# Optimization experiments

Measured on AMD Instinct MI355X. Metric: run time of the kernel, lower is better.

## Reference

```python
import jax, jax.numpy as jnp
import numpy as np

EPS = 1e-5  # torch BatchNorm1d default eps

def _bn(y, gamma, beta):
    # training-mode BatchNorm1d over batch axis (biased variance), per timestep
    mu = jnp.mean(y, axis=0, keepdims=True)
    var = jnp.mean((y - mu) ** 2, axis=0, keepdims=True)
    return gamma * (y - mu) * jax.lax.rsqrt(var + EPS) + beta

def setup_inputs() -> dict:
    key = jax.random.key(0)
    ks = jax.random.split(key, 16)
    T, B, I, H = 512, 64, 512, 512
    s = 1.0 / np.sqrt(H)
    def w(k, shape):
        return jax.random.uniform(k, shape, jnp.float32, -s, s)
    return {
        "x": jax.random.normal(ks[0], (T, B, I), jnp.float32),
        "h0": jnp.zeros((1, B, H), jnp.float32),
        "W_z_w": w(ks[1], (H, H)), "W_z_b": w(ks[2], (H,)),
        "U_z_w": w(ks[3], (H, I)), "U_z_b": w(ks[4], (H,)),
        "W_r_w": w(ks[5], (H, H)), "W_r_b": w(ks[6], (H,)),
        "U_r_w": w(ks[7], (H, I)), "U_r_b": w(ks[8], (H,)),
        "W_h_w": w(ks[9], (H, H)), "W_h_b": w(ks[10], (H,)),
        "U_h_w": w(ks[11], (H, I)), "U_h_b": w(ks[12], (H,)),
        "bn_gamma": jnp.ones((H,), jnp.float32),
        "bn_beta": jnp.zeros((H,), jnp.float32),
    }

def reference(x, h0, W_z_w, W_z_b, U_z_w, U_z_b, W_r_w, W_r_b, U_r_w, U_r_b,
              W_h_w, W_h_b, U_h_w, U_h_b, bn_gamma, bn_beta):
    T, B, _ = x.shape
    H = h0.shape[-1]
    # precompute input projections for all timesteps (parallelizable part)
    uz = jnp.einsum('tbi,hi->tbh', x, U_z_w) + U_z_b  # [T,B,H]
    ur = jnp.einsum('tbi,hi->tbh', x, U_r_w) + U_r_b
    uh = jnp.einsum('tbi,hi->tbh', x, U_h_w) + U_h_b

    def step(h, inp):
        uz_t, ur_t, uh_t = inp
        z = jax.nn.sigmoid(h @ W_z_w.T + W_z_b + _bn(uz_t, bn_gamma, bn_beta))
        r = jax.nn.sigmoid(h @ W_r_w.T + W_r_b + _bn(ur_t, bn_gamma, bn_beta))
        new_state = jnp.tanh((r * h) @ W_h_w.T + W_h_b + _bn(uh_t, bn_gamma, bn_beta))
        h_new = (1.0 - z) * h + z * new_state
        return h_new, h_new

    _, hs = jax.lax.scan(step, h0[0], (uz, ur, uh))  # hs: [T,B,H]
    output = hs.reshape(T, B, 1, H)   # [T, B, directions=1, H]
    h_out = hs.reshape(1, T, B, H)    # faithful to torch code's final `h`
    return output, h_out
```

## Files before the change

kernel.cpp:

```cpp
#include <hip/hip_runtime.h>
#include <hip/hip_bf16.h>


using bf16x8 = __attribute__((ext_vector_type(8))) short;
using f32x4  = __attribute__((ext_vector_type(4))) float;
using fvec4  = __attribute__((ext_vector_type(4))) float;
using s16x4  = __attribute__((ext_vector_type(4))) short;

#define NWG 32

static __device__ __forceinline__ unsigned short f2bf(float f) {
  union { float ff; unsigned int i; } v; v.ff = f;
  unsigned int x = v.i;
  x += 0x7fffu + ((x >> 16) & 1u);
  return (unsigned short)(x >> 16);
}
static __device__ __forceinline__ float h2f(unsigned short u) {
  union { unsigned short s; _Float16 h; } v; v.s = u; return (float)v.h;
}
static __device__ __forceinline__ unsigned short f2h(float f) {
  union { unsigned short s; _Float16 h; } v; v.h = (_Float16)f; return v.s;
}
static __device__ __forceinline__ float sigmoidf_(float x) {
  return 1.0f / (1.0f + __expf(-x));
}
static __device__ __forceinline__ float tanhf_(float x) {
  return 2.0f / (1.0f + __expf(-2.0f * x)) - 1.0f;
}

__global__ __launch_bounds__(256) void proj_gemm(
    const float* __restrict__ x,
    const float* __restrict__ Uz, const float* __restrict__ Ur,
    const float* __restrict__ Uh,
    const float* __restrict__ Wzb, const float* __restrict__ Wrb,
    const float* __restrict__ Whb,
    const float* __restrict__ gamma, const float* __restrict__ beta,
    unsigned short* __restrict__ ubz, unsigned short* __restrict__ ubr,
    unsigned short* __restrict__ ubh)
{
  const int mt = blockIdx.x, nt = blockIdx.y, mat = blockIdx.z;
  const float* U  = (mat == 0) ? Uz  : (mat == 1 ? Ur  : Uh);
  const float* Wb = (mat == 0) ? Wzb : (mat == 1 ? Wrb : Whb);
  unsigned short* uo = (mat == 0) ? ubz : (mat == 1 ? ubr : ubh);

  __shared__ short lA[4096];
  __shared__ short lB[4096];

  const int tid = threadIdx.x;
  const int wave = tid >> 6, lane = tid & 63;
  const int fl = lane & 15, kseg = lane >> 4;

  f32x4 acc[4];
  #pragma unroll
  for (int n = 0; n < 4; ++n) acc[n] = f32x4{0.f, 0.f, 0.f, 0.f};

  const float* xb = x + (size_t)mt * 64 * 512;
  const float* Ub = U + (size_t)nt * 64 * 512;

  for (int kt = 0; kt < 8; ++kt) {
    __syncthreads();
    #pragma unroll
    for (int c = 0; c < 2; ++c) {
      const int chunk = tid + 256 * c;
      const int row = chunk >> 3, kc = chunk & 7;
      const int lb = row * 128 + ((kc * 16) ^ ((row & 7) << 4));
      {
        const float* g = xb + (size_t)row * 512 + kt * 64 + kc * 8;
        fvec4 a0 = *(const fvec4*)g, a1 = *(const fvec4*)(g + 4);
        bf16x8 p;
        p[0] = (short)f2bf(a0[0]); p[1] = (short)f2bf(a0[1]);
        p[2] = (short)f2bf(a0[2]); p[3] = (short)f2bf(a0[3]);
        p[4] = (short)f2bf(a1[0]); p[5] = (short)f2bf(a1[1]);
        p[6] = (short)f2bf(a1[2]); p[7] = (short)f2bf(a1[3]);
        *(bf16x8*)((char*)lA + lb) = p;
      }
      {
        const float* g = Ub + (size_t)row * 512 + kt * 64 + kc * 8;
        fvec4 a0 = *(const fvec4*)g, a1 = *(const fvec4*)(g + 4);
        bf16x8 p;
        p[0] = (short)f2bf(a0[0]); p[1] = (short)f2bf(a0[1]);
        p[2] = (short)f2bf(a0[2]); p[3] = (short)f2bf(a0[3]);
        p[4] = (short)f2bf(a1[0]); p[5] = (short)f2bf(a1[1]);
        p[6] = (short)f2bf(a1[2]); p[7] = (short)f2bf(a1[3]);
        *(bf16x8*)((char*)lB + lb) = p;
      }
    }
    __syncthreads();
    #pragma unroll
    for (int kk = 0; kk < 2; ++kk) {
      const int ar = wave * 16 + fl;
      bf16x8 af = *(const bf16x8*)((char*)lA + ar * 128 +
                    ((kk * 64 + kseg * 16) ^ ((ar & 7) << 4)));
      #pragma unroll
      for (int n = 0; n < 4; ++n) {
        const int br = n * 16 + fl;
        bf16x8 bfr = *(const bf16x8*)((char*)lB + br * 128 +
                      ((kk * 64 + kseg * 16) ^ ((br & 7) << 4)));
        acc[n] = __builtin_amdgcn_mfma_f32_16x16x32_bf16(af, bfr, acc[n], 0, 0, 0);
      }
    }
  }

  float sn[4], qn[4];
  #pragma unroll
  for (int n = 0; n < 4; ++n) {
    sn[n] = acc[n][0] + acc[n][1] + acc[n][2] + acc[n][3];
    qn[n] = acc[n][0]*acc[n][0] + acc[n][1]*acc[n][1]
          + acc[n][2]*acc[n][2] + acc[n][3]*acc[n][3];
    sn[n] += __shfl_xor(sn[n], 16); qn[n] += __shfl_xor(qn[n], 16);
    sn[n] += __shfl_xor(sn[n], 32); qn[n] += __shfl_xor(qn[n], 32);
  }
  __syncthreads();
  float* sArr = (float*)lA;
  float* qArr = (float*)lB;
  if (kseg == 0) {
    #pragma unroll
    for (int n = 0; n < 4; ++n) {
      sArr[wave * 64 + n * 16 + fl] = sn[n];
      qArr[wave * 64 + n * 16 + fl] = qn[n];
    }
  }
  __syncthreads();

  const int c0 = nt * 64;
  const int b0 = wave * 16 + kseg * 4;
  #pragma unroll
  for (int n = 0; n < 4; ++n) {
    const int idx = n * 16 + fl;
    const float s = sArr[idx] + sArr[64+idx] + sArr[128+idx] + sArr[192+idx];
    const float q = qArr[idx] + qArr[64+idx] + qArr[128+idx] + qArr[192+idx];
    const float mu = s * 0.015625f;
    const float rs = rsqrtf(q * 0.015625f - mu * mu + 1e-5f);
    const int col = c0 + idx;
    const float gb  = gamma[col] * rs;
    const float ofs = beta[col] + Wb[col] - gb * mu;
    s16x4 pk;
    #pragma unroll
    for (int i = 0; i < 4; ++i)
      pk[i] = (short)f2h(gb * acc[n][i] + ofs);
    *(s16x4*)(uo + ((size_t)mt * 512 + col) * 64 + b0) = pk;
  }
}

__global__ __launch_bounds__(256) void gru_scan(
    const float* __restrict__ h0,
    const float* __restrict__ Wz, const float* __restrict__ Wr,
    const float* __restrict__ Wh,
    const unsigned short* __restrict__ ubz, const unsigned short* __restrict__ ubr,
    const unsigned short* __restrict__ ubh,
    unsigned short* __restrict__ hbuf, unsigned short* __restrict__ rhbuf,
    unsigned int* __restrict__ flags, float* __restrict__ out)
{
  const int wg = blockIdx.x;
  const int tid = threadIdx.x;
  const int wave = tid >> 6, lane = tid & 63;
  const int fl = lane & 15, kseg = lane >> 4;
  const int col = wg * 16 + fl;
  const int row0 = wave * 16 + kseg * 4;
  const int hrow = wave * 16 + fl;

  __shared__ short lW[24576];

  for (int c = tid; c < 3072; c += 256) {
    const int m = c >> 10, rem = c & 1023;
    const int r = rem >> 6, kc = rem & 63;
    const float* W = (m == 0) ? Wz : (m == 1 ? Wr : Wh);
    const float* g = W + (size_t)(wg * 16 + r) * 512 + kc * 8;
    bf16x8 p;
    #pragma unroll
    for (int j = 0; j < 8; ++j) p[j] = (short)f2bf(g[j]);
    *(bf16x8*)((char*)lW + m * 16384 + r * 1024 + ((kc * 16) ^ ((r & 7) << 4))) = p;
  }

  auto wait_ev = [&](unsigned int ev) {
    if (lane < NWG) {
      while (__hip_atomic_load(&flags[lane << 5], __ATOMIC_RELAXED,
                               __HIP_MEMORY_SCOPE_AGENT) < ev) {}
    }
    __builtin_amdgcn_fence(__ATOMIC_ACQUIRE, "agent");
  };

  float hown[4];
  #pragma unroll
  for (int i = 0; i < 4; ++i) {
    const float v = h0[(size_t)(row0 + i) * 512 + col];
    hown[i] = v;
    hbuf[(size_t)(row0 + i) * 512 + col] = f2bf(v);
  }
  __syncthreads();
  if (tid == 0)
    __hip_atomic_store(&flags[wg << 5], 1u, __ATOMIC_RELEASE, __HIP_MEMORY_SCOPE_AGENT);

  float uzv[4], urv[4], uhv[4];
  {
    const size_t ub = ((size_t)col) * 64 + row0;
    s16x4 az = *(const s16x4*)(ubz + ub);
    s16x4 ar = *(const s16x4*)(ubr + ub);
    s16x4 ah = *(const s16x4*)(ubh + ub);
    #pragma unroll
    for (int i = 0; i < 4; ++i) {
      uzv[i] = h2f((unsigned short)az[i]);
      urv[i] = h2f((unsigned short)ar[i]);
      uhv[i] = h2f((unsigned short)ah[i]);
    }
  }

  for (int t = 0; t < 512; ++t) {
    wait_ev(2 * t + 1);

    bf16x8 af[16];
    #pragma unroll
    for (int kk = 0; kk < 16; ++kk)
      af[kk] = *(const bf16x8*)((const char*)hbuf + hrow * 1024 + kk * 64 + kseg * 16);

    f32x4 zacc = f32x4{0.f,0.f,0.f,0.f}, racc = f32x4{0.f,0.f,0.f,0.f};
    #pragma unroll
    for (int kk = 0; kk < 16; ++kk) {
      const int wof = (kk * 64 + kseg * 16) ^ ((fl & 7) << 4);
      bf16x8 b0 = *(const bf16x8*)((const char*)lW + fl * 1024 + wof);
      bf16x8 b1 = *(const bf16x8*)((const char*)lW + 16384 + fl * 1024 + wof);
      zacc = __builtin_amdgcn_mfma_f32_16x16x32_bf16(af[kk], b0, zacc, 0, 0, 0);
      racc = __builtin_amdgcn_mfma_f32_16x16x32_bf16(af[kk], b1, racc, 0, 0, 0);
    }

    float z4[4], r4[4];
    #pragma unroll
    for (int i = 0; i < 4; ++i) {
      z4[i] = sigmoidf_(zacc[i] + uzv[i]);
      r4[i] = sigmoidf_(racc[i] + urv[i]);
    }

    #pragma unroll
    for (int i = 0; i < 4; ++i)
      rhbuf[(size_t)(row0 + i) * 512 + col] = f2bf(r4[i] * hown[i]);

    __syncthreads();
    if (tid == 0)
      __hip_atomic_store(&flags[wg << 5], 2u * t + 2u, __ATOMIC_RELEASE,
                         __HIP_MEMORY_SCOPE_AGENT);
    wait_ev(2 * t + 2);

    #pragma unroll
    for (int kk = 0; kk < 16; ++kk)
      af[kk] = *(const bf16x8*)((const char*)rhbuf + hrow * 1024 + kk * 64 + kseg * 16);

    f32x4 hacc = f32x4{0.f,0.f,0.f,0.f};
    #pragma unroll
    for (int kk = 0; kk < 16; ++kk) {
      const int wof = (kk * 64 + kseg * 16) ^ ((fl & 7) << 4);
      bf16x8 b2 = *(const bf16x8*)((const char*)lW + 32768 + fl * 1024 + wof);
      hacc = __builtin_amdgcn_mfma_f32_16x16x32_bf16(af[kk], b2, hacc, 0, 0, 0);
    }

    float hn[4];
    #pragma unroll
    for (int i = 0; i < 4; ++i) {
      const float nb = tanhf_(hacc[i] + uhv[i]);
      hn[i] = (1.f - z4[i]) * hown[i] + z4[i] * nb;
      hown[i] = hn[i];
    }
    #pragma unroll
    for (int i = 0; i < 4; ++i)
      hbuf[(size_t)(row0 + i) * 512 + col] = f2bf(hn[i]);

    __syncthreads();
    if (tid == 0)
      __hip_atomic_store(&flags[wg << 5], 2u * t + 3u, __ATOMIC_RELEASE,
                         __HIP_MEMORY_SCOPE_AGENT);

    if (t + 1 < 512) {
      const size_t ub = ((size_t)(t + 1) * 512 + col) * 64 + row0;
      s16x4 az = *(const s16x4*)(ubz + ub);
      s16x4 ar = *(const s16x4*)(ubr + ub);
      s16x4 ah = *(const s16x4*)(ubh + ub);
      #pragma unroll
      for (int i = 0; i < 4; ++i) {
        uzv[i] = h2f((unsigned short)az[i]);
        urv[i] = h2f((unsigned short)ar[i]);
        uhv[i] = h2f((unsigned short)ah[i]);
      }
    }
    {
      const size_t tb = (size_t)t * 64 * 512;
      #pragma unroll
      for (int i = 0; i < 4; ++i) {
        const size_t o = tb + (size_t)(row0 + i) * 512 + col;
        const float v = hn[i];
        out[o] = v;
        out[16777216 + o] = v;
      }
    }
  }
}

extern "C" void kernel_launch(void* const* d_in, const int* in_sizes, int n_in,
                              void* d_out, int out_size, void* d_ws, size_t ws_size,
                              hipStream_t stream) {
  (void)in_sizes; (void)n_in; (void)out_size; (void)ws_size;
  const float* x   = (const float*)d_in[0];
  const float* h0  = (const float*)d_in[1];
  const float* Wz  = (const float*)d_in[2];
  const float* Wzb = (const float*)d_in[3];
  const float* Uz  = (const float*)d_in[4];
  const float* Wr  = (const float*)d_in[6];
  const float* Wrb = (const float*)d_in[7];
  const float* Ur  = (const float*)d_in[8];
  const float* Wh  = (const float*)d_in[10];
  const float* Whb = (const float*)d_in[11];
  const float* Uh  = (const float*)d_in[12];
  const float* gam = (const float*)d_in[14];
  const float* bet = (const float*)d_in[15];
  float* out = (float*)d_out;

  char* ws = (char*)d_ws;
  unsigned int*   flags = (unsigned int*)(ws);
  unsigned short* hbuf  = (unsigned short*)(ws + 8192);
  unsigned short* rhbuf = (unsigned short*)(ws + 8192 + 65536);
  unsigned short* uzb   = (unsigned short*)(ws + 262144);
  unsigned short* urb   = (unsigned short*)(ws + 262144 + 33554432);
  unsigned short* uhb   = (unsigned short*)(ws + 262144 + 2ll * 33554432);

  hipMemsetAsync(flags, 0, 8192, stream);

  dim3 gp(512, 8, 3);
  proj_gemm<<<gp, 256, 0, stream>>>(x, Uz, Ur, Uh, Wzb, Wrb, Whb,
                                    gam, bet, uzb, urb, uhb);
  gru_scan<<<dim3(NWG), 256, 0, stream>>>(h0, Wz, Wr, Wh, uzb, urb, uhb,
                                          hbuf, rhbuf, flags, out);
}
```

Baseline: 5.739 ms.

## Replace acquire/release fences with relaxed agent-scope atomics for grid sync buffers

Shares the hidden-state exchange buffers as packed 32-bit words: neighbouring lanes pair their bf16 values with a shuffle, and only one lane of each pair writes, using relaxed agent-scope atomic stores. Reads use 64-bit relaxed atomic loads, so the data bypasses the non-coherent caches without a full acquire fence. The release on the flag store becomes an explicit vmcnt wait plus a relaxed store, which removes the acquire/release fences and their cache writeback or invalidate in each half-step of the 512-step serial scan. The risk is memory-ordering correctness, since it relies on vmcnt(0) and atomic cache bypass instead of formal release/acquire semantics.

```diff
diff --git a/kernel.cpp b/kernel.cpp
--- a/kernel.cpp
+++ b/kernel.cpp
@@ -148,7 +148,7 @@
     const float* __restrict__ Wh,
     const unsigned short* __restrict__ ubz, const unsigned short* __restrict__ ubr,
     const unsigned short* __restrict__ ubh,
-    unsigned short* __restrict__ hbuf, unsigned short* __restrict__ rhbuf,
+    unsigned int* __restrict__ hbuf, unsigned int* __restrict__ rhbuf,
     unsigned int* __restrict__ flags, float* __restrict__ out)
 {
   const int wg = blockIdx.x;
@@ -172,24 +172,49 @@
     *(bf16x8*)((char*)lW + m * 16384 + r * 1024 + ((kc * 16) ^ ((r & 7) << 4))) = p;
   }
 
+  auto publish4 = [&](unsigned int* buf, const float v0, const float v1,
+                      const float v2, const float v3) {
+    float vv[4] = {v0, v1, v2, v3};
+    #pragma unroll
+    for (int i = 0; i < 4; ++i) {
+      unsigned int mine = f2bf(vv[i]);
+      unsigned int other = (unsigned int)__shfl_xor((int)mine, 1);
+      unsigned int word = (fl & 1) ? ((mine << 16) | other)
+                                   : (mine | (other << 16));
+      if ((fl & 1) == (i & 1))
+        __hip_atomic_store(&buf[(row0 + i) * 256 + (col >> 1)], word,
+                           __ATOMIC_RELAXED, __HIP_MEMORY_SCOPE_AGENT);
+    }
+  };
+  auto read_frag = [&](const unsigned int* buf, int kk) -> bf16x8 {
+    const unsigned long long* p =
+        (const unsigned long long*)buf + hrow * 128 + kk * 8 + kseg * 2;
+    union { unsigned long long q[2]; bf16x8 f; } u;
+    u.q[0] = __hip_atomic_load(p,     __ATOMIC_RELAXED, __HIP_MEMORY_SCOPE_AGENT);
+    u.q[1] = __hip_atomic_load(p + 1, __ATOMIC_RELAXED, __HIP_MEMORY_SCOPE_AGENT);
+    return u.f;
+  };
   auto wait_ev = [&](unsigned int ev) {
     if (lane < NWG) {
       while (__hip_atomic_load(&flags[lane << 5], __ATOMIC_RELAXED,
                                __HIP_MEMORY_SCOPE_AGENT) < ev) {}
     }
-    __builtin_amdgcn_fence(__ATOMIC_ACQUIRE, "agent");
+    asm volatile("" ::: "memory");
+  };
+  auto arrive = [&](unsigned int ev) {
+    asm volatile("s_waitcnt vmcnt(0)" ::: "memory");
+    __syncthreads();
+    if (tid == 0)
+      __hip_atomic_store(&flags[wg << 5], ev, __ATOMIC_RELAXED,
+                         __HIP_MEMORY_SCOPE_AGENT);
   };
 
   float hown[4];
   #pragma unroll
-  for (int i = 0; i < 4; ++i) {
-    const float v = h0[(size_t)(row0 + i) * 512 + col];
-    hown[i] = v;
-    hbuf[(size_t)(row0 + i) * 512 + col] = f2bf(v);
-  }
-  __syncthreads();
-  if (tid == 0)
-    __hip_atomic_store(&flags[wg << 5], 1u, __ATOMIC_RELEASE, __HIP_MEMORY_SCOPE_AGENT);
+  for (int i = 0; i < 4; ++i)
+    hown[i] = h0[(size_t)(row0 + i) * 512 + col];
+  publish4(hbuf, hown[0], hown[1], hown[2], hown[3]);
+  arrive(1u);
 
   float uzv[4], urv[4], uhv[4];
   {
@@ -211,7 +236,7 @@
     bf16x8 af[16];
     #pragma unroll
     for (int kk = 0; kk < 16; ++kk)
-      af[kk] = *(const bf16x8*)((const char*)hbuf + hrow * 1024 + kk * 64 + kseg * 16);
+      af[kk] = read_frag(hbuf, kk);
 
     f32x4 zacc = f32x4{0.f,0.f,0.f,0.f}, racc = f32x4{0.f,0.f,0.f,0.f};
     #pragma unroll
@@ -230,19 +255,15 @@
       r4[i] = sigmoidf_(racc[i] + urv[i]);
     }
 
-    #pragma unroll
-    for (int i = 0; i < 4; ++i)
-      rhbuf[(size_t)(row0 + i) * 512 + col] = f2bf(r4[i] * hown[i]);
-
-    __syncthreads();
-    if (tid == 0)
-      __hip_atomic_store(&flags[wg << 5], 2u * t + 2u, __ATOMIC_RELEASE,
-                         __HIP_MEMORY_SCOPE_AGENT);
+    publish4(rhbuf, r4[0] * hown[0], r4[1] * hown[1],
+                    r4[2] * hown[2], r4[3] * hown[3]);
+
+    arrive(2u * t + 2u);
     wait_ev(2 * t + 2);
 
     #pragma unroll
     for (int kk = 0; kk < 16; ++kk)
-      af[kk] = *(const bf16x8*)((const char*)rhbuf + hrow * 1024 + kk * 64 + kseg * 16);
+      af[kk] = read_frag(rhbuf, kk);
 
     f32x4 hacc = f32x4{0.f,0.f,0.f,0.f};
     #pragma unroll
@@ -259,14 +280,9 @@
       hn[i] = (1.f - z4[i]) * hown[i] + z4[i] * nb;
       hown[i] = hn[i];
     }
-    #pragma unroll
-    for (int i = 0; i < 4; ++i)
-      hbuf[(size_t)(row0 + i) * 512 + col] = f2bf(hn[i]);
-
-    __syncthreads();
-    if (tid == 0)
-      __hip_atomic_store(&flags[wg << 5], 2u * t + 3u, __ATOMIC_RELEASE,
-                         __HIP_MEMORY_SCOPE_AGENT);
+    publish4(hbuf, hn[0], hn[1], hn[2], hn[3]);
+
+    arrive(2u * t + 3u);
 
     if (t + 1 < 512) {
       const size_t ub = ((size_t)(t + 1) * 512 + col) * 64 + row0;
@@ -314,8 +330,8 @@
 
   char* ws = (char*)d_ws;
   unsigned int*   flags = (unsigned int*)(ws);
-  unsigned short* hbuf  = (unsigned short*)(ws + 8192);
-  unsigned short* rhbuf = (unsigned short*)(ws + 8192 + 65536);
+  unsigned int*   hbuf  = (unsigned int*)(ws + 8192);
+  unsigned int*   rhbuf = (unsigned int*)(ws + 8192 + 65536);
   unsigned short* uzb   = (unsigned short*)(ws + 262144);
   unsigned short* urb   = (unsigned short*)(ws + 262144 + 33554432);
   unsigned short* uhb   = (unsigned short*)(ws + 262144 + 2ll * 33554432);
```

Measured after the change: 5.885 ms. +2.6%, slower.

## Split GRU scan by batch to drop cross-workgroup flag synchronisation

Applied to the files above, without the earlier changes.

The recurrent scan now runs on 4 workgroups of 512 threads, each owning 16 batch rows and all 512 hidden columns. This replaces the 32 column-split workgroups that exchanged h and r*h through global buffers and spin-waited on atomic flags twice per step. h and r*h now stay in shared memory. The recurrent weights are converted to bf16 once by a new kernel and are streamed from global memory/L2 every step instead of being held in LDS. The uh projection is parked in a not-yet-written tail region of the output buffer to save workspace. The trade-off is that per-step MFMA work is concentrated on only 4 CUs and each CU must re-read about 1.5 MB of weights per timestep from L2.

```diff
diff --git a/kernel.cpp b/kernel.cpp
--- a/kernel.cpp
+++ b/kernel.cpp
@@ -6,8 +6,6 @@
 using f32x4  = __attribute__((ext_vector_type(4))) float;
 using fvec4  = __attribute__((ext_vector_type(4))) float;
 using s16x4  = __attribute__((ext_vector_type(4))) short;
-
-#define NWG 32
 
 static __device__ __forceinline__ unsigned short f2bf(float f) {
   union { float ff; unsigned int i; } v; v.ff = f;
@@ -26,6 +24,35 @@
 }
 static __device__ __forceinline__ float tanhf_(float x) {
   return 2.0f / (1.0f + __expf(-2.0f * x)) - 1.0f;
+}
+
+static __device__ __forceinline__ size_t uh_off(int tp, int col, int b0) {
+  const int wg = b0 >> 4, bu = b0 & 15;
+  const int idx = ((tp & 1) << 14) + col * 32 + bu * 2;
+  return (size_t)100663296u + (size_t)(tp >> 1) * 131072u
+       + (size_t)(wg * 16 + (idx >> 11)) * 2048u + (size_t)(idx & 2047);
+}
+
+__global__ __launch_bounds__(256) void wconv(
+    const float* __restrict__ a, const float* __restrict__ b,
+    const float* __restrict__ c,
+    unsigned short* __restrict__ oa, unsigned short* __restrict__ ob,
+    unsigned short* __restrict__ oc)
+{
+  const int i = (blockIdx.x * 256 + threadIdx.x) * 4;
+  fvec4 va = *(const fvec4*)(a + i);
+  fvec4 vb = *(const fvec4*)(b + i);
+  fvec4 vc = *(const fvec4*)(c + i);
+  s16x4 pa, pb, pc;
+  #pragma unroll
+  for (int j = 0; j < 4; ++j) {
+    pa[j] = (short)f2bf(va[j]);
+    pb[j] = (short)f2bf(vb[j]);
+    pc[j] = (short)f2bf(vc[j]);
+  }
+  *(s16x4*)(oa + i) = pa;
+  *(s16x4*)(ob + i) = pb;
+  *(s16x4*)(oc + i) = pc;
 }
 
 __global__ __launch_bounds__(256) void proj_gemm(
@@ -36,12 +63,11 @@
     const float* __restrict__ Whb,
     const float* __restrict__ gamma, const float* __restrict__ beta,
     unsigned short* __restrict__ ubz, unsigned short* __restrict__ ubr,
-    unsigned short* __restrict__ ubh)
+    float* __restrict__ outb)
 {
   const int mt = blockIdx.x, nt = blockIdx.y, mat = blockIdx.z;
   const float* U  = (mat == 0) ? Uz  : (mat == 1 ? Ur  : Uh);
   const float* Wb = (mat == 0) ? Wzb : (mat == 1 ? Wrb : Whb);
-  unsigned short* uo = (mat == 0) ? ubz : (mat == 1 ? ubr : ubh);
 
   __shared__ short lA[4096];
   __shared__ short lB[4096];
@@ -138,158 +164,187 @@
     #pragma unroll
     for (int i = 0; i < 4; ++i)
       pk[i] = (short)f2h(gb * acc[n][i] + ofs);
-    *(s16x4*)(uo + ((size_t)mt * 512 + col) * 64 + b0) = pk;
-  }
-}
-
-__global__ __launch_bounds__(256) void gru_scan(
+    if (mat == 2) {
+      *(s16x4*)((char*)outb + uh_off(mt, col, b0)) = pk;
+    } else {
+      unsigned short* uo = (mat == 0) ? ubz : ubr;
+      *(s16x4*)(uo + ((size_t)mt * 512 + col) * 64 + b0) = pk;
+    }
+  }
+}
+
+__global__ __launch_bounds__(512) void gru_scan(
     const float* __restrict__ h0,
-    const float* __restrict__ Wz, const float* __restrict__ Wr,
-    const float* __restrict__ Wh,
+    const unsigned short* __restrict__ wz, const unsigned short* __restrict__ wr,
+    const unsigned short* __restrict__ wh,
     const unsigned short* __restrict__ ubz, const unsigned short* __restrict__ ubr,
-    const unsigned short* __restrict__ ubh,
-    unsigned short* __restrict__ hbuf, unsigned short* __restrict__ rhbuf,
-    unsigned int* __restrict__ flags, float* __restrict__ out)
+    float* __restrict__ out)
 {
   const int wg = blockIdx.x;
   const int tid = threadIdx.x;
   const int wave = tid >> 6, lane = tid & 63;
-  const int fl = lane & 15, kseg = lane >> 4;
-  const int col = wg * 16 + fl;
-  const int row0 = wave * 16 + kseg * 4;
-  const int hrow = wave * 16 + fl;
-
-  __shared__ short lW[24576];
-
-  for (int c = tid; c < 3072; c += 256) {
-    const int m = c >> 10, rem = c & 1023;
-    const int r = rem >> 6, kc = rem & 63;
-    const float* W = (m == 0) ? Wz : (m == 1 ? Wr : Wh);
-    const float* g = W + (size_t)(wg * 16 + r) * 512 + kc * 8;
-    bf16x8 p;
-    #pragma unroll
-    for (int j = 0; j < 8; ++j) p[j] = (short)f2bf(g[j]);
-    *(bf16x8*)((char*)lW + m * 16384 + r * 1024 + ((kc * 16) ^ ((r & 7) << 4))) = p;
-  }
-
-  auto wait_ev = [&](unsigned int ev) {
-    if (lane < NWG) {
-      while (__hip_atomic_load(&flags[lane << 5], __ATOMIC_RELAXED,
-                               __HIP_MEMORY_SCOPE_AGENT) < ev) {}
-    }
-    __builtin_amdgcn_fence(__ATOMIC_ACQUIRE, "agent");
-  };
-
-  float hown[4];
-  #pragma unroll
-  for (int i = 0; i < 4; ++i) {
-    const float v = h0[(size_t)(row0 + i) * 512 + col];
-    hown[i] = v;
-    hbuf[(size_t)(row0 + i) * 512 + col] = f2bf(v);
+  const int fl = lane & 15, ks = lane >> 4;
+  const int n0 = wave * 64;
+
+  __shared__ short lh[8192];
+  __shared__ short lrh[8192];
+
+  float hown[4][4];
+  #pragma unroll
+  for (int nt = 0; nt < 4; ++nt) {
+    const int col = n0 + nt * 16 + fl;
+    #pragma unroll
+    for (int i = 0; i < 4; ++i) {
+      const int b = ks * 4 + i;
+      const float v = h0[(size_t)(wg * 16 + b) * 512 + col];
+      hown[nt][i] = v;
+      *(short*)((char*)lh + b * 1024 + ((col * 2) ^ ((b & 7) << 4))) =
+          (short)f2bf(v);
+    }
   }
   __syncthreads();
-  if (tid == 0)
-    __hip_atomic_store(&flags[wg << 5], 1u, __ATOMIC_RELEASE, __HIP_MEMORY_SCOPE_AGENT);
-
-  float uzv[4], urv[4], uhv[4];
-  {
-    const size_t ub = ((size_t)col) * 64 + row0;
-    s16x4 az = *(const s16x4*)(ubz + ub);
-    s16x4 ar = *(const s16x4*)(ubr + ub);
-    s16x4 ah = *(const s16x4*)(ubh + ub);
-    #pragma unroll
-    for (int i = 0; i < 4; ++i) {
-      uzv[i] = h2f((unsigned short)az[i]);
-      urv[i] = h2f((unsigned short)ar[i]);
-      uhv[i] = h2f((unsigned short)ah[i]);
-    }
-  }
+
+  s16x4 ucz[4], ucr[4], uch[4];
+  #pragma unroll
+  for (int nt = 0; nt < 4; ++nt) {
+    const int col = n0 + nt * 16 + fl;
+    const size_t o = ((size_t)col) * 64 + wg * 16 + ks * 4;
+    ucz[nt] = *(const s16x4*)(ubz + o);
+    ucr[nt] = *(const s16x4*)(ubr + o);
+    uch[nt] = *(const s16x4*)((const char*)out + uh_off(0, col, wg * 16 + ks * 4));
+  }
+
+  const unsigned short* Wab[2] = {wz, wr};
 
   for (int t = 0; t < 512; ++t) {
-    wait_ev(2 * t + 1);
-
-    bf16x8 af[16];
+    bf16x8 A[16];
     #pragma unroll
     for (int kk = 0; kk < 16; ++kk)
-      af[kk] = *(const bf16x8*)((const char*)hbuf + hrow * 1024 + kk * 64 + kseg * 16);
-
-    f32x4 zacc = f32x4{0.f,0.f,0.f,0.f}, racc = f32x4{0.f,0.f,0.f,0.f};
-    #pragma unroll
-    for (int kk = 0; kk < 16; ++kk) {
-      const int wof = (kk * 64 + kseg * 16) ^ ((fl & 7) << 4);
-      bf16x8 b0 = *(const bf16x8*)((const char*)lW + fl * 1024 + wof);
-      bf16x8 b1 = *(const bf16x8*)((const char*)lW + 16384 + fl * 1024 + wof);
-      zacc = __builtin_amdgcn_mfma_f32_16x16x32_bf16(af[kk], b0, zacc, 0, 0, 0);
-      racc = __builtin_amdgcn_mfma_f32_16x16x32_bf16(af[kk], b1, racc, 0, 0, 0);
-    }
-
-    float z4[4], r4[4];
-    #pragma unroll
-    for (int i = 0; i < 4; ++i) {
-      z4[i] = sigmoidf_(zacc[i] + uzv[i]);
-      r4[i] = sigmoidf_(racc[i] + urv[i]);
-    }
-
-    #pragma unroll
-    for (int i = 0; i < 4; ++i)
-      rhbuf[(size_t)(row0 + i) * 512 + col] = f2bf(r4[i] * hown[i]);
-
+      A[kk] = *(const bf16x8*)((const char*)lh + fl * 1024 +
+                ((kk * 64 + ks * 16) ^ ((fl & 7) << 4)));
+
+    f32x4 ga[2][4];
+    #pragma unroll
+    for (int m = 0; m < 2; ++m)
+      #pragma unroll
+      for (int n = 0; n < 4; ++n) ga[m][n] = f32x4{0.f, 0.f, 0.f, 0.f};
+
+    bf16x8 Pa[8], Pb[8];
+    {
+      const unsigned short* bp = Wab[0] + ((n0 + fl) * 512 + ks * 8);
+      #pragma unroll
+      for (int j = 0; j < 8; ++j) Pa[j] = *(const bf16x8*)(bp + j * 32);
+    }
+    #pragma unroll
+    for (int hb = 0; hb < 16; ++hb) {
+      if (hb + 1 < 16) {
+        const int h2 = hb + 1;
+        const int m2 = h2 >> 3, nt2 = (h2 >> 1) & 3, hf2 = h2 & 1;
+        const unsigned short* bp =
+            Wab[m2] + ((n0 + nt2 * 16 + fl) * 512 + hf2 * 256 + ks * 8);
+        bf16x8* nxt = (hb & 1) ? Pa : Pb;
+        #pragma unroll
+        for (int j = 0; j < 8; ++j) nxt[j] = *(const bf16x8*)(bp + j * 32);
+      }
+      bf16x8* cur = (hb & 1) ? Pb : Pa;
+      const int mat = hb >> 3, nt = (hb >> 1) & 3, half = hb & 1;
+      #pragma unroll
+      for (int j = 0; j < 8; ++j)
+        ga[mat][nt] = __builtin_amdgcn_mfma_f32_16x16x32_bf16(
+            A[half * 8 + j], cur[j], ga[mat][nt], 0, 0, 0);
+    }
+
+    float z4[4][4];
+    #pragma unroll
+    for (int nt = 0; nt < 4; ++nt) {
+      const int col = n0 + nt * 16 + fl;
+      #pragma unroll
+      for (int i = 0; i < 4; ++i) {
+        const float z = sigmoidf_(ga[0][nt][i] + h2f((unsigned short)ucz[nt][i]));
+        const float r = sigmoidf_(ga[1][nt][i] + h2f((unsigned short)ucr[nt][i]));
+        z4[nt][i] = z;
+        const int b = ks * 4 + i;
+        *(short*)((char*)lrh + b * 1024 + ((col * 2) ^ ((b & 7) << 4))) =
+            (short)f2bf(r * hown[nt][i]);
+      }
+    }
     __syncthreads();
-    if (tid == 0)
-      __hip_atomic_store(&flags[wg << 5], 2u * t + 2u, __ATOMIC_RELEASE,
-                         __HIP_MEMORY_SCOPE_AGENT);
-    wait_ev(2 * t + 2);
-
+
+    bf16x8 A2[16];
     #pragma unroll
     for (int kk = 0; kk < 16; ++kk)
-      af[kk] = *(const bf16x8*)((const char*)rhbuf + hrow * 1024 + kk * 64 + kseg * 16);
-
-    f32x4 hacc = f32x4{0.f,0.f,0.f,0.f};
-    #pragma unroll
-    for (int kk = 0; kk < 16; ++kk) {
-      const int wof = (kk * 64 + kseg * 16) ^ ((fl & 7) << 4);
-      bf16x8 b2 = *(const bf16x8*)((const char*)lW + 32768 + fl * 1024 + wof);
-      hacc = __builtin_amdgcn_mfma_f32_16x16x32_bf16(af[kk], b2, hacc, 0, 0, 0);
-    }
-
-    float hn[4];
-    #pragma unroll
-    for (int i = 0; i < 4; ++i) {
-      const float nb = tanhf_(hacc[i] + uhv[i]);
-      hn[i] = (1.f - z4[i]) * hown[i] + z4[i] * nb;
-      hown[i] = hn[i];
-    }
-    #pragma unroll
-    for (int i = 0; i < 4; ++i)
-      hbuf[(size_t)(row0 + i) * 512 + col] = f2bf(hn[i]);
-
+      A2[kk] = *(const bf16x8*)((const char*)lrh + fl * 1024 +
+                 ((kk * 64 + ks * 16) ^ ((fl & 7) << 4)));
+
+    f32x4 hc[4];
+    #pragma unroll
+    for (int n = 0; n < 4; ++n) hc[n] = f32x4{0.f, 0.f, 0.f, 0.f};
+
+    {
+      const unsigned short* bp = wh + ((n0 + fl) * 512 + ks * 8);
+      #pragma unroll
+      for (int j = 0; j < 8; ++j) Pa[j] = *(const bf16x8*)(bp + j * 32);
+    }
+    #pragma unroll
+    for (int hb = 0; hb < 8; ++hb) {
+      if (hb + 1 < 8) {
+        const int h2 = hb + 1;
+        const int nt2 = h2 >> 1, hf2 = h2 & 1;
+        const unsigned short* bp =
+            wh + ((n0 + nt2 * 16 + fl) * 512 + hf2 * 256 + ks * 8);
+        bf16x8* nxt = (hb & 1) ? Pa : Pb;
+        #pragma unroll
+        for (int j = 0; j < 8; ++j) nxt[j] = *(const bf16x8*)(bp + j * 32);
+      }
+      bf16x8* cur = (hb & 1) ? Pb : Pa;
+      const int nt = hb >> 1, half = hb & 1;
+      #pragma unroll
+      for (int j = 0; j < 8; ++j)
+        hc[nt] = __builtin_amdgcn_mfma_f32_16x16x32_bf16(
+            A2[half * 8 + j], cur[j], hc[nt], 0, 0, 0);
+    }
+
+    if (t + 1 < 512) {
+      #pragma unroll
+      for (int nt = 0; nt < 4; ++nt) {
+        const int col = n0 + nt * 16 + fl;
+        const size_t o = ((size_t)(t + 1) * 512 + col) * 64 + wg * 16 + ks * 4;
+        ucz[nt] = *(const s16x4*)(ubz + o);
+        ucr[nt] = *(const s16x4*)(ubr + o);
+        uch_nxt_guard:;
+      }
+    }
+    s16x4 uhn[4];
+    if (t + 1 < 512) {
+      #pragma unroll
+      for (int nt = 0; nt < 4; ++nt) {
+        const int col = n0 + nt * 16 + fl;
+        uhn[nt] = *(const s16x4*)((const char*)out +
+                    uh_off(t + 1, col, wg * 16 + ks * 4));
+      }
+    }
+
+    #pragma unroll
+    for (int nt = 0; nt < 4; ++nt) {
+      const int col = n0 + nt * 16 + fl;
+      #pragma unroll
+      for (int i = 0; i < 4; ++i) {
+        const float nb = tanhf_(hc[nt][i] + h2f((unsigned short)uch[nt][i]));
+        const float hn = (1.f - z4[nt][i]) * hown[nt][i] + z4[nt][i] * nb;
+        hown[nt][i] = hn;
+        const int b = ks * 4 + i;
+        *(short*)((char*)lh + b * 1024 + ((col * 2) ^ ((b & 7) << 4))) =
+            (short)f2bf(hn);
+        const size_t o = ((size_t)t * 64 + wg * 16 + b) * 512 + col;
+        out[o] = hn;
+        out[16777216 + o] = hn;
+      }
+    }
+    if (t + 1 < 512) {
+      #pragma unroll
+      for (int nt = 0; nt < 4; ++nt) uch[nt] = uhn[nt];
+    }
     __syncthreads();
-    if (tid == 0)
-      __hip_atomic_store(&flags[wg << 5], 2u * t + 3u, __ATOMIC_RELEASE,
-                         __HIP_MEMORY_SCOPE_AGENT);
-
-    if (t + 1 < 512) {
-      const size_t ub = ((size_t)(t + 1) * 512 + col) * 64 + row0;
-      s16x4 az = *(const s16x4*)(ubz + ub);
-      s16x4 ar = *(const s16x4*)(ubr + ub);
-      s16x4 ah = *(const s16x4*)(ubh + ub);
-      #pragma unroll
-      for (int i = 0; i < 4; ++i) {
-        uzv[i] = h2f((unsigned short)az[i]);
-        urv[i] = h2f((unsigned short)ar[i]);
-        uhv[i] = h2f((unsigned short)ah[i]);
-      }
-    }
-    {
-      const size_t tb = (size_t)t * 64 * 512;
-      #pragma unroll
-      for (int i = 0; i < 4; ++i) {
-        const size_t o = tb + (size_t)(row0 + i) * 512 + col;
-        const float v = hn[i];
-        out[o] = v;
-        out[16777216 + o] = v;
-      }
-    }
   }
 }
 
@@ -313,18 +368,15 @@
   float* out = (float*)d_out;
 
   char* ws = (char*)d_ws;
-  unsigned int*   flags = (unsigned int*)(ws);
-  unsigned short* hbuf  = (unsigned short*)(ws + 8192);
-  unsigned short* rhbuf = (unsigned short*)(ws + 8192 + 65536);
-  unsigned short* uzb   = (unsigned short*)(ws + 262144);
-  unsigned short* urb   = (unsigned short*)(ws + 262144 + 33554432);
-  unsigned short* uhb   = (unsigned short*)(ws + 262144 + 2ll * 33554432);
-
-  hipMemsetAsync(flags, 0, 8192, stream);
-
+  unsigned short* wz16 = (unsigned short*)(ws);
+  unsigned short* wr16 = (unsigned short*)(ws + 524288);
+  unsigned short* wh16 = (unsigned short*)(ws + 1048576);
+  unsigned short* uzb  = (unsigned short*)(ws + 1572864);
+  unsigned short* urb  = (unsigned short*)(ws + 1572864 + 33554432);
+
+  wconv<<<dim3(256), 256, 0, stream>>>(Wz, Wr, Wh, wz16, wr16, wh16);
   dim3 gp(512, 8, 3);
   proj_gemm<<<gp, 256, 0, stream>>>(x, Uz, Ur, Uh, Wzb, Wrb, Whb,
-                                    gam, bet, uzb, urb, uhb);
-  gru_scan<<<dim3(NWG), 256, 0, stream>>>(h0, Wz, Wr, Wh, uzb, urb, uhb,
-                                          hbuf, rhbuf, flags, out);
-}
+                                    gam, bet, uzb, urb, out);
+  gru_scan<<<dim3(4), 512, 0, stream>>>(h0, wz16, wr16, wh16, uzb, urb, out);
+}
```

New measurement: 21.88 ms. 281% more time.
